# Performance work log

Hardware: AMD Instinct MI355X
Metric: run time of the kernel (lower is better)

## Reference

```python
import jax, jax.numpy as jnp
import numpy as np

B, L, HID, H = 2, 2048, 1024, 16
HD = HID // H
MAX_REL = 2


def setup_inputs() -> dict:
    key = jax.random.key(0)
    ks = jax.random.split(key, 16)
    s = 0.02
    return {
        "query": jax.random.normal(ks[0], (B, L, HID), jnp.float32),
        "key": jax.random.normal(ks[1], (B, L, HID), jnp.float32),
        "value": jax.random.normal(ks[2], (B, L, HID), jnp.float32),
        "Wq": jax.random.normal(ks[3], (HID, HID), jnp.float32) * s,
        "bq": jnp.zeros((HID,), jnp.float32),
        "Wk": jax.random.normal(ks[4], (HID, HID), jnp.float32) * s,
        "bk": jnp.zeros((HID,), jnp.float32),
        "Wv": jax.random.normal(ks[5], (HID, HID), jnp.float32) * s,
        "bv": jnp.zeros((HID,), jnp.float32),
        "Wo": jax.random.normal(ks[6], (HID, HID), jnp.float32) * s,
        "bo": jnp.zeros((HID,), jnp.float32),
        "rel_k_table": jax.random.normal(ks[7], (2 * MAX_REL + 1, HD), jnp.float32) * s,
        "rel_v_table": jax.random.normal(ks[8], (2 * MAX_REL + 1, HD), jnp.float32) * s,
    }


def _rel_embeddings(table, len_q, len_k):
    # Shaw-style clipped relative position lookup -> [len_q, len_k, head_dim]
    dist = jnp.arange(len_k)[None, :] - jnp.arange(len_q)[:, None]
    idx = jnp.clip(dist, -MAX_REL, MAX_REL) + MAX_REL
    return table[idx]


def reference(query, key, value, Wq, bq, Wk, bk, Wv, bv, Wo, bo, rel_k_table, rel_v_table):
    b, lq, hid = query.shape
    lk = key.shape[1]
    q = (query @ Wq.T + bq).reshape(b, lq, H, HD)   # [b, lq, h, hd]
    k = (key @ Wk.T + bk).reshape(b, lk, H, HD)     # [b, lk, h, hd]
    v = (value @ Wv.T + bv).reshape(b, lk, H, HD)   # [b, lk, h, hd]

    rk = _rel_embeddings(rel_k_table, lq, lk)       # [lq, lk, hd]
    rv = _rel_embeddings(rel_v_table, lq, lk)       # [lq, lk, hd]

    attn1 = jnp.einsum('bqhd,bkhd->bhqk', q, k)
    attn2 = jnp.einsum('bqhd,qkd->bhqk', q, rk)
    # NOTE: original code averages the two scores and does NOT divide by sqrt(head_dim)
    attn = jax.nn.softmax((attn1 + attn2) * 0.5, axis=-1)

    w1 = jnp.einsum('bhqk,bkhd->bhqd', attn, v)
    w2 = jnp.einsum('bhqk,qkd->bhqd', attn, rv)
    x = (w1 + w2).transpose(0, 2, 1, 3).reshape(b, lq, hid)
    return x @ Wo.T + bo
```

## Files before the change

### kernel.cpp

```cpp
#include <hip/hip_runtime.h>
#include <hip/hip_bf16.h>
#include <math.h>

typedef __attribute__((ext_vector_type(8))) short bf16x8;
typedef __attribute__((ext_vector_type(4))) float f32x4;
typedef __attribute__((ext_vector_type(16))) float f32x16;

constexpr int Bc   = 2;
constexpr int Lc   = 2048;
constexpr int HIDc = 1024;
constexpr int Hc   = 16;
constexpr int HDc  = 64;
constexpr int Mc   = 4096;

__device__ __forceinline__ ushort f2bf(float f) {
  uint u = __float_as_uint(f);
  u += 0x7fff + ((u >> 16) & 1);
  return (ushort)(u >> 16);
}

__device__ __forceinline__ void gload16(const ushort* g, ushort* l) {
  __builtin_amdgcn_global_load_lds(
      (const __attribute__((address_space(1))) uint*)(const void*)g,
      (__attribute__((address_space(3))) uint*)(void*)l, 16, 0, 0);
}

__device__ __forceinline__ uint cvtpk(float lo, float hi_) {
  uint r;
  asm("v_cvt_pk_bf16_f32 %0, %1, %2" : "=v"(r) : "v"(lo), "v"(hi_));
  return r;
}
__device__ __forceinline__ void pswap(uint &a, uint &b) {
  asm("v_permlane32_swap_b32 %0, %1" : "+v"(a), "+v"(b));
}

template<int MODE>
__device__ __forceinline__ void gemm_core(
    const float* __restrict__ A, const float* __restrict__ Bw,
    const float* __restrict__ bias, float* __restrict__ Cf,
    ushort* __restrict__ Cb, int tile,
    ushort (*As)[2048], ushort (*Bs)[4096])
{
  const int tid  = threadIdx.x;
  const int lane = tid & 63;
  const int w    = tid >> 6;
  const int g    = lane >> 4;
  const int lc   = lane & 15;
  const int wr   = w >> 2;
  const int wc   = w & 3;
  const int row0 = (tile >> 3) * 64;
  const int col0 = (tile & 7) * 128;

  const int sr  = tid >> 2;
  const int sc_ = tid & 3;
  const int wofs = sr*32 + (sc_ ^ ((sr >> 1) & 3))*8;
  const float* pA = A  + (size_t)(row0 + sr) * HIDc + sc_*8;
  const float* pB = Bw + (size_t)(col0 + sr) * HIDc + sc_*8;

  int aoff[2], boff[2];
  #pragma unroll
  for (int mi = 0; mi < 2; ++mi) {
    int r = wr*32 + mi*16 + lc;
    aoff[mi] = r*32 + (g ^ ((r >> 1) & 3)) * 8;
  }
  #pragma unroll
  for (int ni = 0; ni < 2; ++ni) {
    int r = wc*32 + ni*16 + lc;
    boff[ni] = r*32 + (g ^ ((r >> 1) & 3)) * 8;
  }

  f32x4 acc[2][2];
  #pragma unroll
  for (int mi = 0; mi < 2; ++mi)
    #pragma unroll
    for (int ni = 0; ni < 2; ++ni) acc[mi][ni] = (f32x4){0.f,0.f,0.f,0.f};

  float4 a0, a1, b0, b1;
  auto ld = [&](int ko) {
    b0 = *(const float4*)(pB + ko);
    b1 = *(const float4*)(pB + ko + 4);
    if (tid < 256) {
      a0 = *(const float4*)(pA + ko);
      a1 = *(const float4*)(pA + ko + 4);
    }
  };
  auto wrbuf = [&](int bi) {
    ushort tb[8] = { f2bf(b0.x), f2bf(b0.y), f2bf(b0.z), f2bf(b0.w),
                     f2bf(b1.x), f2bf(b1.y), f2bf(b1.z), f2bf(b1.w) };
    *(uint4*)&Bs[bi][wofs] = *(uint4*)tb;
    if (tid < 256) {
      ushort ta[8] = { f2bf(a0.x), f2bf(a0.y), f2bf(a0.z), f2bf(a0.w),
                       f2bf(a1.x), f2bf(a1.y), f2bf(a1.z), f2bf(a1.w) };
      *(uint4*)&As[bi][wofs] = *(uint4*)ta;
    }
  };

  ld(0); wrbuf(0);
  __syncthreads();

  for (int t = 0; t < 32; ++t) {
    if (t < 31) ld((t + 1) * 32);
    const ushort* as = As[t & 1];
    const ushort* bs = Bs[t & 1];
    bf16x8 af[2], bfr[2];
    #pragma unroll
    for (int mi = 0; mi < 2; ++mi) af[mi] = *(const bf16x8*)&as[aoff[mi]];
    #pragma unroll
    for (int ni = 0; ni < 2; ++ni) bfr[ni] = *(const bf16x8*)&bs[boff[ni]];
    #pragma unroll
    for (int mi = 0; mi < 2; ++mi)
      #pragma unroll
      for (int ni = 0; ni < 2; ++ni)
        acc[mi][ni] = __builtin_amdgcn_mfma_f32_16x16x32_bf16(af[mi], bfr[ni], acc[mi][ni], 0, 0, 0);
    if (t < 31) wrbuf((t + 1) & 1);
    __syncthreads();
  }

  const int colbase = col0 + wc*32;
  if (MODE == 0) {
    #pragma unroll
    for (int mi = 0; mi < 2; ++mi) {
      int row = row0 + wr*32 + mi*16 + 4*g;
      #pragma unroll
      for (int ni = 0; ni < 2; ++ni) {
        int col = colbase + ni*16 + lc;
        float bb = bias[col];
        #pragma unroll
        for (int reg = 0; reg < 4; ++reg)
          Cf[(size_t)(row + reg) * HIDc + col] = acc[mi][ni][reg] + bb;
      }
    }
  } else if (MODE == 1) {
    #pragma unroll
    for (int mi = 0; mi < 2; ++mi) {
      int row = row0 + wr*32 + mi*16 + 4*g;
      int b = row >> 11, qq = row & 2047;
      #pragma unroll
      for (int ni = 0; ni < 2; ++ni) {
        int col = colbase + ni*16 + lc;
        int h = col >> 6, d = col & 63;
        float bb = bias[col];
        size_t base = (((size_t)b*Hc + h)*Lc + qq)*HDc + d;
        #pragma unroll
        for (int reg = 0; reg < 4; ++reg)
          Cb[base + (size_t)reg*HDc] = f2bf(acc[mi][ni][reg] + bb);
      }
    }
  } else {
    #pragma unroll
    for (int mi = 0; mi < 2; ++mi) {
      int row = row0 + wr*32 + mi*16 + 4*g;
      int b = row >> 11, kk = row & 2047;
      #pragma unroll
      for (int ni = 0; ni < 2; ++ni) {
        int col = colbase + ni*16 + lc;
        int h = col >> 6, d = col & 63;
        float bb = bias[col];
        ushort t4[4];
        #pragma unroll
        for (int reg = 0; reg < 4; ++reg) t4[reg] = f2bf(acc[mi][ni][reg] + bb);
        *(uint2*)&Cb[(((size_t)b*Hc + h)*HDc + d)*Lc + kk] = *(uint2*)t4;
      }
    }
  }
}

__global__ __launch_bounds__(512)
void gemm_fused(const float* __restrict__ q, const float* __restrict__ k,
                const float* __restrict__ v,
                const float* __restrict__ Wq, const float* __restrict__ Wk,
                const float* __restrict__ Wv,
                const float* __restrict__ bq, const float* __restrict__ bk,
                const float* __restrict__ bv,
                ushort* Qc, ushort* Kc, ushort* Vt)
{
  __shared__ ushort As[2][2048];
  __shared__ ushort Bs[2][4096];
  int gi   = blockIdx.x >> 9;
  int tile = blockIdx.x & 511;
  if (gi == 0)      gemm_core<1>(q, Wq, bq, nullptr, Qc, tile, As, Bs);
  else if (gi == 1) gemm_core<1>(k, Wk, bk, nullptr, Kc, tile, As, Bs);
  else              gemm_core<2>(v, Wv, bv, nullptr, Vt, tile, As, Bs);
}

__global__ __launch_bounds__(512)
void gemm_out(const float* __restrict__ X, const float* __restrict__ Wo,
              const float* __restrict__ bo, float* __restrict__ out)
{
  __shared__ ushort As[2][2048];
  __shared__ ushort Bs[2][4096];
  gemm_core<0>(X, Wo, bo, out, nullptr, blockIdx.x, As, Bs);
}

__global__ __launch_bounds__(128)
void attn_mfma32(const ushort* __restrict__ Qc, const ushort* __restrict__ Kc,
                 const ushort* __restrict__ Vt, const float* __restrict__ relk,
                 const float* __restrict__ relv, float* __restrict__ X)
{
  __shared__ ushort KVs[2][4608];

  const int tid  = threadIdx.x;
  const int w    = tid >> 6;
  const int lane = tid & 63;
  const int lq   = lane & 31;
  const int hi   = lane >> 5;

  const int swz  = (blockIdx.x & 7) * 128 + (blockIdx.x >> 3);
  const int qblk = swz & 31;
  const int bh   = swz >> 5;
  const int b    = bh >> 4;
  const int h    = bh & 15;
  const int qw   = qblk*64 + w*32;
  const int qabs = qw + lq;

  constexpr float C2 = 0.72134752f;

  const ushort* Kbh = Kc + (size_t)bh*Lc*HDc;
  const ushort* Vbh = Vt + (size_t)bh*HDc*Lc;

  bf16x8 qf[4];
  const ushort* qbase = Qc + ((size_t)bh*Lc + qabs)*HDc + 8*hi;
  #pragma unroll
  for (int s = 0; s < 4; ++s) qf[s] = *(const bf16x8*)(qbase + 16*s);

  f32x16 dc;
  #pragma unroll
  for (int i = 0; i < 16; ++i) dc[i] = 0.f;
  #pragma unroll
  for (int s = 0; s < 4; ++s) {
    union { ushort u[8]; bf16x8 v; } rf;
    #pragma unroll
    for (int j = 0; j < 8; ++j) rf.u[j] = 0;
    if (lq < 5) {
      #pragma unroll
      for (int j = 0; j < 8; ++j) rf.u[j] = f2bf(relk[lq*HDc + 16*s + 8*hi + j]);
    }
    dc = __builtin_amdgcn_mfma_f32_32x32x16_bf16(rf.v, qf[s], dc, 0, 0, 0);
  }
  float o0 = __shfl_xor(dc[0], 32), o1 = __shfl_xor(dc[1], 32),
        o2 = __shfl_xor(dc[2], 32), o3 = __shfl_xor(dc[3], 32);
  float dqh0, dqh1, dqh2, dqh3, dqh4;
  if (hi == 0) { dqh0 = dc[0]; dqh1 = dc[1]; dqh2 = dc[2]; dqh3 = dc[3]; dqh4 = o0; }
  else         { dqh0 = o0;    dqh1 = o1;    dqh2 = o2;    dqh3 = o3;    dqh4 = dc[0]; }
  dqh0 *= C2; dqh1 *= C2; dqh2 *= C2; dqh3 *= C2; dqh4 *= C2;

  f32x16 acc0, acc1;
  #pragma unroll
  for (int i = 0; i < 16; ++i) { acc0[i] = 0.f; acc1[i] = 0.f; }
  float lsum = 0.f, llo = 0.f, e1 = 0.f, e2 = 0.f, e3 = 0.f;

  auto stage = [&](ushort* dst, int k0) {
    #pragma unroll
    for (int seg = 0; seg < 5; ++seg) {
      int widx = seg*2 + w;
      if (widx < 5) {
        int vc = widx*64 + lane;
        int row = vc/5, ch = vc - row*5;
        gload16(Vbh + (size_t)row*Lc + k0 + ch*8, dst + vc*8);
      } else if (widx < 9) {
        int kc = (widx - 5)*64 + lane;
        int row = kc >> 3, pch = kc & 7;
        int gch = pch ^ (row & 7);
        gload16(Kbh + (size_t)(k0 + row)*HDc + gch*8, dst + (320 + kc)*8);
      }
    }
  };

  stage(KVs[0], 0);
  __syncthreads();

  for (int t = 0; t < Lc/32; ++t) {
    const ushort* vb_ = KVs[t & 1];
    const ushort* kb_ = vb_ + 2560;
    if (t + 1 < Lc/32) stage(KVs[(t+1) & 1], (t+1)*32);
    const int kb = t*32;

    bf16x8 kfa[4];
    #pragma unroll
    for (int s = 0; s < 4; ++s)
      kfa[s] = *(const bf16x8*)&kb_[lq*64 + ((2*s + hi) ^ (lq & 7))*8];
    f32x16 c0;
    #pragma unroll
    for (int i = 0; i < 16; ++i) c0[i] = 0.f;
    __builtin_amdgcn_s_setprio(1);
    #pragma unroll
    for (int s = 0; s < 4; ++s)
      c0 = __builtin_amdgcn_mfma_f32_32x32x16_bf16(kfa[s], qf[s], c0, 0, 0, 0);
    __builtin_amdgcn_s_setprio(0);

    bf16x8 vf00 = *(const bf16x8*)&vb_[lq*40      + hi*8];
    bf16x8 vf01 = *(const bf16x8*)&vb_[(32+lq)*40 + hi*8];
    bf16x8 vf10 = *(const bf16x8*)&vb_[lq*40      + (2+hi)*8];
    bf16x8 vf11 = *(const bf16x8*)&vb_[(32+lq)*40 + (2+hi)*8];

    uint pk[8];
    const bool allhi = (kb >= qw + 33);
    const bool alllo = (kb + 33 <= qw);
    if (allhi | alllo) {
      const float dq = allhi ? dqh4 : dqh0;
      float gs = 0.f;
      #pragma unroll
      for (int jj = 0; jj < 8; ++jj) {
        float pa = __builtin_amdgcn_exp2f(__builtin_fmaf(c0[2*jj],   C2, dq));
        float pb = __builtin_amdgcn_exp2f(__builtin_fmaf(c0[2*jj+1], C2, dq));
        gs += pa + pb;
        pk[jj] = cvtpk(pa, pb);
      }
      lsum += gs;
      if (alllo) llo += gs;
    } else {
      int bnum = kb + 4*hi - qabs;
      #pragma unroll
      for (int jj = 0; jj < 8; ++jj) {
        int r0 = 2*jj;
        int d0 = bnum + ((r0 & 3) + 8*(r0 >> 2));
        int d1 = d0 + 1;
        float dqa = d0 <= -2 ? dqh0 : (d0 >= 2 ? dqh4 :
                    (d0 == -1 ? dqh1 : (d0 == 0 ? dqh2 : dqh3)));
        float dqb = d1 <= -2 ? dqh0 : (d1 >= 2 ? dqh4 :
                    (d1 == -1 ? dqh1 : (d1 == 0 ? dqh2 : dqh3)));
        float pa = __builtin_amdgcn_exp2f(__builtin_fmaf(c0[r0],   C2, dqa));
        float pb = __builtin_amdgcn_exp2f(__builtin_fmaf(c0[r0+1], C2, dqb));
        lsum += pa + pb;
        llo += (d0 <= -2 ? pa : 0.f) + (d1 <= -2 ? pb : 0.f);
        e1  += (d0 == -1 ? pa : 0.f) + (d1 == -1 ? pb : 0.f);
        e2  += (d0 ==  0 ? pa : 0.f) + (d1 ==  0 ? pb : 0.f);
        e3  += (d0 ==  1 ? pa : 0.f) + (d1 ==  1 ? pb : 0.f);
        pk[jj] = cvtpk(pa, pb);
      }
    }

    uint X0 = pk[0], X1 = pk[1], Y0 = pk[2], Y1 = pk[3];
    pswap(X0, Y0); pswap(X1, Y1);
    union { uint u[4]; bf16x8 v; } aw0;
    aw0.u[0] = X0; aw0.u[1] = X1; aw0.u[2] = Y0; aw0.u[3] = Y1;
    X0 = pk[4]; X1 = pk[5]; Y0 = pk[6]; Y1 = pk[7];
    pswap(X0, Y0); pswap(X1, Y1);
    union { uint u[4]; bf16x8 v; } aw1;
    aw1.u[0] = X0; aw1.u[1] = X1; aw1.u[2] = Y0; aw1.u[3] = Y1;
    __builtin_amdgcn_s_setprio(1);
    acc0 = __builtin_amdgcn_mfma_f32_32x32x16_bf16(aw0.v, vf00, acc0, 0, 0, 0);
    acc1 = __builtin_amdgcn_mfma_f32_32x32x16_bf16(aw0.v, vf01, acc1, 0, 0, 0);
    acc0 = __builtin_amdgcn_mfma_f32_32x32x16_bf16(aw1.v, vf10, acc0, 0, 0, 0);
    acc1 = __builtin_amdgcn_mfma_f32_32x32x16_bf16(aw1.v, vf11, acc1, 0, 0, 0);
    __builtin_amdgcn_s_setprio(0);
    __syncthreads();
  }

  float Ls = lsum + __shfl_xor(lsum, 32);
  float Lo = llo  + __shfl_xor(llo, 32);
  float E1 = e1   + __shfl_xor(e1, 32);
  float E2 = e2   + __shfl_xor(e2, 32);
  float E3 = e3   + __shfl_xor(e3, 32);
  float inv = 1.f / Ls;
  float s0v = Lo*inv, s1v = E1*inv, s2v = E2*inv, s3v = E3*inv;
  float s4v = 1.f - s0v - s1v - s2v - s3v;

  float rvv[5][2];
  #pragma unroll
  for (int r = 0; r < 5; ++r) {
    rvv[r][0] = relv[r*HDc + lq];
    rvv[r][1] = relv[r*HDc + 32 + lq];
  }
  #pragma unroll
  for (int r = 0; r < 16; ++r) {
    int qloc = ((r & 3) + 8*(r >> 2)) + 4*hi;
    float iv = __shfl(inv, qloc);
    float t0 = __shfl(s0v, qloc);
    float t1 = __shfl(s1v, qloc);
    float t2 = __shfl(s2v, qloc);
    float t3 = __shfl(s3v, qloc);
    float t4 = __shfl(s4v, qloc);
    size_t rowb = ((size_t)(b*Lc + qw + qloc))*HIDc + h*HDc;
    X[rowb + lq]      = acc0[r]*iv + t0*rvv[0][0] + t1*rvv[1][0] + t2*rvv[2][0]
                      + t3*rvv[3][0] + t4*rvv[4][0];
    X[rowb + 32 + lq] = acc1[r]*iv + t0*rvv[0][1] + t1*rvv[1][1] + t2*rvv[2][1]
                      + t3*rvv[3][1] + t4*rvv[4][1];
  }
}

extern "C" void kernel_launch(void* const* d_in, const int* in_sizes, int n_in,
                              void* d_out, int out_size, void* d_ws, size_t ws_size,
                              hipStream_t stream) {
  const float* query = (const float*)d_in[0];
  const float* key   = (const float*)d_in[1];
  const float* value = (const float*)d_in[2];
  const float* Wq    = (const float*)d_in[3];
  const float* bq    = (const float*)d_in[4];
  const float* Wk    = (const float*)d_in[5];
  const float* bk    = (const float*)d_in[6];
  const float* Wv    = (const float*)d_in[7];
  const float* bv    = (const float*)d_in[8];
  const float* Wo    = (const float*)d_in[9];
  const float* bo    = (const float*)d_in[10];
  const float* relk  = (const float*)d_in[11];
  const float* relv  = (const float*)d_in[12];
  float* out = (float*)d_out;

  size_t S = (size_t)Bc * Hc * Lc * HDc;
  ushort* Qc = (ushort*)d_ws;
  ushort* Kc = Qc + S;
  ushort* Vt = Kc + S;
  float*  Xb = (float*)(Vt + S);

  gemm_fused<<<3*512, 512, 0, stream>>>(query, key, value, Wq, Wk, Wv,
                                        bq, bk, bv, Qc, Kc, Vt);

  attn_mfma32<<<Bc * Hc * (Lc / 64), 128, 0, stream>>>(Qc, Kc, Vt, relk, relv, Xb);

  gemm_out<<<512, 512, 0, stream>>>(Xb, Wo, bo, out);
}
```

Before: 178.4 us.

## Split attention key range across two wave pairs and merge partials in LDS

The attention block grows from 2 to 4 waves. Each pair of waves processes half of the key sequence into its own double-buffered LDS staging area, so each wave runs half as many loop iterations. Afterwards the second pair writes its partial accumulators and softmax sums to shared memory, and the first pair adds them in before the epilogue. This raises the number of resident waves to hide latency, at the cost of doubled LDS per block, an extra reduction step, and idle waves during the epilogue. The merge is a plain sum, which relies on the softmax accumulation not using a running max.

Result: no change. 178.7 us (+0.2%).

```diff
diff --git a/kernel.cpp b/kernel.cpp
--- a/kernel.cpp
+++ b/kernel.cpp
@@ -192,15 +192,17 @@
   gemm_core<0>(X, Wo, bo, out, nullptr, blockIdx.x, As, Bs);
 }
 
-__global__ __launch_bounds__(128)
+__global__ __launch_bounds__(256)
 void attn_mfma32(const ushort* __restrict__ Qc, const ushort* __restrict__ Kc,
                  const ushort* __restrict__ Vt, const float* __restrict__ relk,
                  const float* __restrict__ relv, float* __restrict__ X)
 {
-  __shared__ ushort KVs[2][4608];
+  __shared__ ushort KVs[2][2][4608];
 
   const int tid  = threadIdx.x;
   const int w    = tid >> 6;
+  const int wp   = w & 1;
+  const int p    = w >> 1;
   const int lane = tid & 63;
   const int lq   = lane & 31;
   const int hi   = lane >> 5;
@@ -210,8 +212,9 @@
   const int bh   = swz >> 5;
   const int b    = bh >> 4;
   const int h    = bh & 15;
-  const int qw   = qblk*64 + w*32;
+  const int qw   = qblk*64 + wp*32;
   const int qabs = qw + lq;
+  const int kbase = p * (Lc/2);
 
   constexpr float C2 = 0.72134752f;
 
@@ -252,7 +255,7 @@
   auto stage = [&](ushort* dst, int k0) {
     #pragma unroll
     for (int seg = 0; seg < 5; ++seg) {
-      int widx = seg*2 + w;
+      int widx = seg*2 + wp;
       if (widx < 5) {
         int vc = widx*64 + lane;
         int row = vc/5, ch = vc - row*5;
@@ -266,14 +269,14 @@
     }
   };
 
-  stage(KVs[0], 0);
+  stage(KVs[p][0], kbase);
   __syncthreads();
 
-  for (int t = 0; t < Lc/32; ++t) {
-    const ushort* vb_ = KVs[t & 1];
+  for (int t = 0; t < Lc/64; ++t) {
+    const ushort* vb_ = KVs[p][t & 1];
     const ushort* kb_ = vb_ + 2560;
-    if (t + 1 < Lc/32) stage(KVs[(t+1) & 1], (t+1)*32);
-    const int kb = t*32;
+    if (t + 1 < Lc/64) stage(KVs[p][(t+1) & 1], kbase + (t+1)*32);
+    const int kb = kbase + t*32;
 
     bf16x8 kfa[4];
     #pragma unroll
@@ -345,6 +348,23 @@
     acc1 = __builtin_amdgcn_mfma_f32_32x32x16_bf16(aw1.v, vf11, acc1, 0, 0, 0);
     __builtin_amdgcn_s_setprio(0);
     __syncthreads();
+  }
+
+  float* sm = (float*)&KVs[0][0][0];
+  if (p == 1) {
+    float* dst = sm + (wp*64 + lane)*38;
+    #pragma unroll
+    for (int i = 0; i < 16; ++i) { dst[i] = acc0[i]; dst[16+i] = acc1[i]; }
+    dst[32] = lsum; dst[33] = llo; dst[34] = e1; dst[35] = e2; dst[36] = e3;
+  }
+  __syncthreads();
+  if (p == 1) return;
+
+  {
+    const float* src = sm + (wp*64 + lane)*38;
+    #pragma unroll
+    for (int i = 0; i < 16; ++i) { acc0[i] += src[i]; acc1[i] += src[16+i]; }
+    lsum += src[32]; llo += src[33]; e1 += src[34]; e2 += src[35]; e3 += src[36];
   }
 
   float Ls = lsum + __shfl_xor(lsum, 32);
@@ -406,7 +426,7 @@
   gemm_fused<<<3*512, 512, 0, stream>>>(query, key, value, Wq, Wk, Wv,
                                         bq, bk, bv, Qc, Kc, Vt);
 
-  attn_mfma32<<<Bc * Hc * (Lc / 64), 128, 0, stream>>>(Qc, Kc, Vt, relk, relv, Xb);
+  attn_mfma32<<<Bc * Hc * (Lc / 64), 256, 0, stream>>>(Qc, Kc, Vt, relk, relv, Xb);
 
   gemm_out<<<512, 512, 0, stream>>>(Xb, Wo, bo, out);
 }
```

## Give each wave a private K/V double buffer and drop block barriers

Applied to the files above, without the earlier changes.

The attention kernel now gives each of the two waves its own double-buffered LDS region for K/V tiles, so each wave stages the full tile itself and waits on its own loads with s_waitcnt vmcnt(0) instead of a per-iteration __syncthreads. Global-load offsets are precomputed once outside the loop, and the loop is unrolled by two to ping-pong the buffers. Fragments are read from LDS before the next tile is issued, which avoids overwriting data still being read. The cost is twice the global/L2 load traffic for K/V and double the LDS footprint per block, which may lower occupancy.

Measured after the change: 183.2 us. 2.7% more time.

```diff
diff --git a/kernel.cpp b/kernel.cpp
--- a/kernel.cpp
+++ b/kernel.cpp
@@ -197,7 +197,7 @@
                  const ushort* __restrict__ Vt, const float* __restrict__ relk,
                  const float* __restrict__ relv, float* __restrict__ X)
 {
-  __shared__ ushort KVs[2][4608];
+  __shared__ ushort KVs[2][2][4608];
 
   const int tid  = threadIdx.x;
   const int w    = tid >> 6;
@@ -249,49 +249,53 @@
   for (int i = 0; i < 16; ++i) { acc0[i] = 0.f; acc1[i] = 0.f; }
   float lsum = 0.f, llo = 0.f, e1 = 0.f, e2 = 0.f, e3 = 0.f;
 
+  uint voffs[5], koffs[4];
+  #pragma unroll
+  for (int i = 0; i < 5; ++i) {
+    int vc = i*64 + lane;
+    int row = vc/5, ch = vc - row*5;
+    voffs[i] = (uint)(row*Lc + ch*8);
+  }
+  #pragma unroll
+  for (int i = 0; i < 4; ++i) {
+    int kc = i*64 + lane;
+    int row = kc >> 3, pch = kc & 7;
+    koffs[i] = (uint)(row*HDc + (pch ^ (row & 7))*8);
+  }
+
   auto stage = [&](ushort* dst, int k0) {
     #pragma unroll
-    for (int seg = 0; seg < 5; ++seg) {
-      int widx = seg*2 + w;
-      if (widx < 5) {
-        int vc = widx*64 + lane;
-        int row = vc/5, ch = vc - row*5;
-        gload16(Vbh + (size_t)row*Lc + k0 + ch*8, dst + vc*8);
-      } else if (widx < 9) {
-        int kc = (widx - 5)*64 + lane;
-        int row = kc >> 3, pch = kc & 7;
-        int gch = pch ^ (row & 7);
-        gload16(Kbh + (size_t)(k0 + row)*HDc + gch*8, dst + (320 + kc)*8);
-      }
-    }
+    for (int i = 0; i < 5; ++i)
+      gload16(Vbh + voffs[i] + k0, dst + i*512 + lane*8);
+    #pragma unroll
+    for (int i = 0; i < 4; ++i)
+      gload16(Kbh + koffs[i] + k0*HDc, dst + 2560 + i*512 + lane*8);
   };
 
-  stage(KVs[0], 0);
-  __syncthreads();
-
-  for (int t = 0; t < Lc/32; ++t) {
-    const ushort* vb_ = KVs[t & 1];
+  auto tileproc = [&](const ushort* vb_, ushort* nxt, int t) {
+    asm volatile("s_waitcnt vmcnt(0)" ::: "memory");
     const ushort* kb_ = vb_ + 2560;
-    if (t + 1 < Lc/32) stage(KVs[(t+1) & 1], (t+1)*32);
     const int kb = t*32;
 
     bf16x8 kfa[4];
     #pragma unroll
     for (int s = 0; s < 4; ++s)
       kfa[s] = *(const bf16x8*)&kb_[lq*64 + ((2*s + hi) ^ (lq & 7))*8];
-    f32x16 c0;
-    #pragma unroll
-    for (int i = 0; i < 16; ++i) c0[i] = 0.f;
-    __builtin_amdgcn_s_setprio(1);
-    #pragma unroll
-    for (int s = 0; s < 4; ++s)
-      c0 = __builtin_amdgcn_mfma_f32_32x32x16_bf16(kfa[s], qf[s], c0, 0, 0, 0);
-    __builtin_amdgcn_s_setprio(0);
-
     bf16x8 vf00 = *(const bf16x8*)&vb_[lq*40      + hi*8];
     bf16x8 vf01 = *(const bf16x8*)&vb_[(32+lq)*40 + hi*8];
     bf16x8 vf10 = *(const bf16x8*)&vb_[lq*40      + (2+hi)*8];
     bf16x8 vf11 = *(const bf16x8*)&vb_[(32+lq)*40 + (2+hi)*8];
+
+    if (t + 1 < Lc/32) stage(nxt, (t+1)*32);
+
+    f32x16 c0;
+    #pragma unroll
+    for (int i = 0; i < 16; ++i) c0[i] = 0.f;
+    __builtin_amdgcn_s_setprio(1);
+    #pragma unroll
+    for (int s = 0; s < 4; ++s)
+      c0 = __builtin_amdgcn_mfma_f32_32x32x16_bf16(kfa[s], qf[s], c0, 0, 0, 0);
+    __builtin_amdgcn_s_setprio(0);
 
     uint pk[8];
     const bool allhi = (kb >= qw + 33);
@@ -344,7 +348,14 @@
     acc0 = __builtin_amdgcn_mfma_f32_32x32x16_bf16(aw1.v, vf10, acc0, 0, 0, 0);
     acc1 = __builtin_amdgcn_mfma_f32_32x32x16_bf16(aw1.v, vf11, acc1, 0, 0, 0);
     __builtin_amdgcn_s_setprio(0);
-    __syncthreads();
+  };
+
+  ushort* buf0 = &KVs[w][0][0];
+  ushort* buf1 = &KVs[w][1][0];
+  stage(buf0, 0);
+  for (int t = 0; t < Lc/32; t += 2) {
+    tileproc(buf0, buf1, t);
+    tileproc(buf1, buf0, t + 1);
   }
 
   float Ls = lsum + __shfl_xor(lsum, 32);
```

## Replace LDS-staged K/V tiles with direct register double-buffered global loads

Applied to the files above, without the earlier changes.

The attention kernel no longer stages K and V tiles through shared memory with global_load_lds and per-iteration barriers. Each wave now loads its K and V MFMA fragments straight from global memory into registers, ping-ponging two register buffers so the next tile's loads are in flight while the current one computes. Blocks grow to 4 waves covering 128 queries, and the grid halves. This removes the barrier and LDS round trip, but every wave now fetches K/V on its own, relying on L2/L1 to absorb the duplicate traffic, and the extra fragment registers may cut occupancy.

Result: slower. 218.8 us (+22.7%).

```diff
diff --git a/kernel.cpp b/kernel.cpp
--- a/kernel.cpp
+++ b/kernel.cpp
@@ -17,12 +17,6 @@
   uint u = __float_as_uint(f);
   u += 0x7fff + ((u >> 16) & 1);
   return (ushort)(u >> 16);
-}
-
-__device__ __forceinline__ void gload16(const ushort* g, ushort* l) {
-  __builtin_amdgcn_global_load_lds(
-      (const __attribute__((address_space(1))) uint*)(const void*)g,
-      (__attribute__((address_space(3))) uint*)(void*)l, 16, 0, 0);
 }
 
 __device__ __forceinline__ uint cvtpk(float lo, float hi_) {
@@ -192,25 +186,23 @@
   gemm_core<0>(X, Wo, bo, out, nullptr, blockIdx.x, As, Bs);
 }
 
-__global__ __launch_bounds__(128)
-void attn_mfma32(const ushort* __restrict__ Qc, const ushort* __restrict__ Kc,
-                 const ushort* __restrict__ Vt, const float* __restrict__ relk,
-                 const float* __restrict__ relv, float* __restrict__ X)
+__global__ __launch_bounds__(256)
+void attn_reg(const ushort* __restrict__ Qc, const ushort* __restrict__ Kc,
+              const ushort* __restrict__ Vt, const float* __restrict__ relk,
+              const float* __restrict__ relv, float* __restrict__ X)
 {
-  __shared__ ushort KVs[2][4608];
-
   const int tid  = threadIdx.x;
   const int w    = tid >> 6;
   const int lane = tid & 63;
   const int lq   = lane & 31;
   const int hi   = lane >> 5;
 
-  const int swz  = (blockIdx.x & 7) * 128 + (blockIdx.x >> 3);
-  const int qblk = swz & 31;
-  const int bh   = swz >> 5;
+  const int swz  = (blockIdx.x & 7) * 64 + (blockIdx.x >> 3);
+  const int qblk = swz & 15;
+  const int bh   = swz >> 4;
   const int b    = bh >> 4;
   const int h    = bh & 15;
-  const int qw   = qblk*64 + w*32;
+  const int qw   = qblk*128 + w*32;
   const int qabs = qw + lq;
 
   constexpr float C2 = 0.72134752f;
@@ -249,49 +241,31 @@
   for (int i = 0; i < 16; ++i) { acc0[i] = 0.f; acc1[i] = 0.f; }
   float lsum = 0.f, llo = 0.f, e1 = 0.f, e2 = 0.f, e3 = 0.f;
 
-  auto stage = [&](ushort* dst, int k0) {
-    #pragma unroll
-    for (int seg = 0; seg < 5; ++seg) {
-      int widx = seg*2 + w;
-      if (widx < 5) {
-        int vc = widx*64 + lane;
-        int row = vc/5, ch = vc - row*5;
-        gload16(Vbh + (size_t)row*Lc + k0 + ch*8, dst + vc*8);
-      } else if (widx < 9) {
-        int kc = (widx - 5)*64 + lane;
-        int row = kc >> 3, pch = kc & 7;
-        int gch = pch ^ (row & 7);
-        gload16(Kbh + (size_t)(k0 + row)*HDc + gch*8, dst + (320 + kc)*8);
-      }
-    }
-  };
-
-  stage(KVs[0], 0);
-  __syncthreads();
-
-  for (int t = 0; t < Lc/32; ++t) {
-    const ushort* vb_ = KVs[t & 1];
-    const ushort* kb_ = vb_ + 2560;
-    if (t + 1 < Lc/32) stage(KVs[(t+1) & 1], (t+1)*32);
-    const int kb = t*32;
-
-    bf16x8 kfa[4];
-    #pragma unroll
-    for (int s = 0; s < 4; ++s)
-      kfa[s] = *(const bf16x8*)&kb_[lq*64 + ((2*s + hi) ^ (lq & 7))*8];
+  const ushort* kp  = Kbh + (size_t)lq*HDc + 8*hi;
+  const ushort* vp0 = Vbh + (size_t)lq*Lc + 8*hi;
+  const ushort* vp1 = Vbh + (size_t)(32 + lq)*Lc + 8*hi;
+
+  auto loadK = [&](int k0, bf16x8* kf) {
+    const ushort* p = kp + (size_t)k0*HDc;
+    #pragma unroll
+    for (int s = 0; s < 4; ++s) kf[s] = *(const bf16x8*)(p + 16*s);
+  };
+  auto loadV = [&](int k0, bf16x8* vf) {
+    vf[0] = *(const bf16x8*)(vp0 + k0);
+    vf[1] = *(const bf16x8*)(vp1 + k0);
+    vf[2] = *(const bf16x8*)(vp0 + k0 + 16);
+    vf[3] = *(const bf16x8*)(vp1 + k0 + 16);
+  };
+
+  auto compute = [&](const bf16x8* kf, const bf16x8* vf, int kb) {
     f32x16 c0;
     #pragma unroll
     for (int i = 0; i < 16; ++i) c0[i] = 0.f;
     __builtin_amdgcn_s_setprio(1);
     #pragma unroll
     for (int s = 0; s < 4; ++s)
-      c0 = __builtin_amdgcn_mfma_f32_32x32x16_bf16(kfa[s], qf[s], c0, 0, 0, 0);
+      c0 = __builtin_amdgcn_mfma_f32_32x32x16_bf16(kf[s], qf[s], c0, 0, 0, 0);
     __builtin_amdgcn_s_setprio(0);
-
-    bf16x8 vf00 = *(const bf16x8*)&vb_[lq*40      + hi*8];
-    bf16x8 vf01 = *(const bf16x8*)&vb_[(32+lq)*40 + hi*8];
-    bf16x8 vf10 = *(const bf16x8*)&vb_[lq*40      + (2+hi)*8];
-    bf16x8 vf11 = *(const bf16x8*)&vb_[(32+lq)*40 + (2+hi)*8];
 
     uint pk[8];
     const bool allhi = (kb >= qw + 33);
@@ -339,12 +313,25 @@
     union { uint u[4]; bf16x8 v; } aw1;
     aw1.u[0] = X0; aw1.u[1] = X1; aw1.u[2] = Y0; aw1.u[3] = Y1;
     __builtin_amdgcn_s_setprio(1);
-    acc0 = __builtin_amdgcn_mfma_f32_32x32x16_bf16(aw0.v, vf00, acc0, 0, 0, 0);
-    acc1 = __builtin_amdgcn_mfma_f32_32x32x16_bf16(aw0.v, vf01, acc1, 0, 0, 0);
-    acc0 = __builtin_amdgcn_mfma_f32_32x32x16_bf16(aw1.v, vf10, acc0, 0, 0, 0);
-    acc1 = __builtin_amdgcn_mfma_f32_32x32x16_bf16(aw1.v, vf11, acc1, 0, 0, 0);
+    acc0 = __builtin_amdgcn_mfma_f32_32x32x16_bf16(aw0.v, vf[0], acc0, 0, 0, 0);
+    acc1 = __builtin_amdgcn_mfma_f32_32x32x16_bf16(aw0.v, vf[1], acc1, 0, 0, 0);
+    acc0 = __builtin_amdgcn_mfma_f32_32x32x16_bf16(aw1.v, vf[2], acc0, 0, 0, 0);
+    acc1 = __builtin_amdgcn_mfma_f32_32x32x16_bf16(aw1.v, vf[3], acc1, 0, 0, 0);
     __builtin_amdgcn_s_setprio(0);
-    __syncthreads();
+  };
+
+  bf16x8 kfA[4], vfA[4], kfB[4], vfB[4];
+  loadK(0, kfA);
+  loadV(0, vfA);
+  for (int t = 0; t < Lc/32; t += 2) {
+    loadK((t+1)*32, kfB);
+    loadV((t+1)*32, vfB);
+    compute(kfA, vfA, t*32);
+    if (t + 2 < Lc/32) {
+      loadK((t+2)*32, kfA);
+      loadV((t+2)*32, vfA);
+    }
+    compute(kfB, vfB, (t+1)*32);
   }
 
   float Ls = lsum + __shfl_xor(lsum, 32);
@@ -406,7 +393,7 @@
   gemm_fused<<<3*512, 512, 0, stream>>>(query, key, value, Wq, Wk, Wv,
                                         bq, bk, bv, Qc, Kc, Vt);
 
-  attn_mfma32<<<Bc * Hc * (Lc / 64), 128, 0, stream>>>(Qc, Kc, Vt, relk, relv, Xb);
+  attn_reg<<<512, 256, 0, stream>>>(Qc, Kc, Vt, relk, relv, Xb);
 
   gemm_out<<<512, 512, 0, stream>>>(Xb, Wo, bo, out);
 }
```
